# Kernel tuning notes

Measured on AMD Instinct MI355X. Metric: run time of the kernel, lower is better.

Reference implementation:

```python
import jax, jax.numpy as jnp
import numpy as np
import math

B, N, D, H, T = 256, 512, 512, 8, 128
HD = D // H
CLIP = 10.0
CAP = 1.0
NEG = -1.0e9


def setup_inputs() -> dict:
    key = jax.random.key(0)
    ks = jax.random.split(key, 12)
    s = 1.0 / math.sqrt(D)
    return {
        "embeddings": jax.random.normal(ks[0], (B, N, D), jnp.float32),
        "mean_graph_emb": jax.random.normal(ks[1], (B, D), jnp.float32),
        "used_capacity": jax.random.uniform(ks[2], (T, B), jnp.float32),
        "Wk": jax.random.normal(ks[3], (D, D), jnp.float32) * s,
        "Wk_tanh": jax.random.normal(ks[4], (D, D), jnp.float32) * s,
        "Wv": jax.random.normal(ks[5], (D, D), jnp.float32) * s,
        "Wq_context": jax.random.normal(ks[6], (D, D), jnp.float32) * s,
        "Wq_step": jax.random.normal(ks[7], (D + 1, D), jnp.float32) * s,
        "Wout": jax.random.normal(ks[8], (D, D), jnp.float32) * s,
        "prev_a": jax.random.randint(ks[9], (T, B), 0, N, jnp.int32),
        "mask": jax.random.randint(ks[10], (T, B, N), 0, 2, jnp.int32),
    }


def reference(embeddings, mean_graph_emb, used_capacity, Wk, Wk_tanh, Wv,
              Wq_context, Wq_step, Wout, prev_a, mask):
    # Projections (done once per graph embedding, as in get_projections)
    K = (embeddings @ Wk).reshape(B, N, H, HD).transpose(0, 2, 1, 3)      # [B,H,N,hd]
    V = (embeddings @ Wv).reshape(B, N, H, HD).transpose(0, 2, 1, 3)      # [B,H,N,hd]
    K_tanh = embeddings @ Wk_tanh                                          # [B,N,D]
    Q_context = mean_graph_emb @ Wq_context                                # [B,D]

    inv_sqrt_hd = 1.0 / math.sqrt(HD)
    inv_sqrt_d = 1.0 / math.sqrt(D)

    def step(carry, xs):
        prev_t, cap_t, mask_t = xs  # [B], [B], [B,N]
        # get_step_context: gather prev node embedding + remaining capacity
        cur_emb = jnp.take_along_axis(embeddings, prev_t[:, None, None], axis=1)[:, 0]  # [B,D]
        step_ctx = jnp.concatenate([cur_emb, (CAP - cap_t)[:, None]], axis=-1)          # [B,D+1]
        q = Q_context + step_ctx @ Wq_step                                               # [B,D]
        qh = q.reshape(B, H, HD)                                                          # [B,H,hd]
        # decoder MHA, seq_len_q = 1
        logits = jnp.einsum("bhd,bhnd->bhn", qh, K) * inv_sqrt_hd                        # [B,H,N]
        logits = jnp.where(mask_t[:, None, :] == 1, NEG, logits)
        attn = jax.nn.softmax(logits, axis=-1)
        mha = jnp.einsum("bhn,bhnd->bhd", attn, V).reshape(B, D) @ Wout                  # [B,D]
        # single-head tanh-clipped pointer logits
        comp = jnp.einsum("bd,bnd->bn", mha, K_tanh) * inv_sqrt_d                        # [B,N]
        comp = jnp.tanh(comp) * CLIP
        comp = jnp.where(mask_t == 1, NEG, comp)
        p = jax.nn.softmax(comp, axis=-1)                                                # [B,N]
        return carry, p

    _, ps = jax.lax.scan(step, None, (prev_a, used_capacity, mask))  # [T,B,N]
    return ps.transpose(1, 0, 2)  # [B,T,N]
```

## Files before the change

kernel.cpp:

```cpp
#include <hip/hip_runtime.h>
#include <hip/hip_bf16.h>

constexpr int Bb = 256;
constexpr int Nn = 512;
constexpr int Dd = 512;
constexpr int Hh = 8;
constexpr int Tt = 128;
#define NEGF (-1.0e9f)

typedef __attribute__((ext_vector_type(4))) float f32x4;
typedef __attribute__((ext_vector_type(8))) short bf16x8;
typedef __attribute__((ext_vector_type(8))) unsigned short u16x8;

#define AS1 __attribute__((address_space(1)))
#define AS3 __attribute__((address_space(3)))

__device__ __forceinline__ unsigned short f2bf(float f) {
  union { float f; unsigned u; } v; v.f = f;
  unsigned r = v.u + 0x7fffu + ((v.u >> 16) & 1u);
  return (unsigned short)(r >> 16);
}

__device__ __forceinline__ unsigned cvtpk(float lo, float hi) {
  unsigned r;
  asm("v_cvt_pk_bf16_f32 %0, %1, %2" : "=v"(r) : "v"(lo), "v"(hi));
  return r;
}

__device__ __forceinline__ void cast8(const float* __restrict__ src,
                                      unsigned short* __restrict__ dst, int i) {
  const float4* s = (const float4*)src + (size_t)i * 2;
  float4 a = s[0], b = s[1];
  u16x8 o;
  o[0] = f2bf(a.x); o[1] = f2bf(a.y); o[2] = f2bf(a.z); o[3] = f2bf(a.w);
  o[4] = f2bf(b.x); o[5] = f2bf(b.y); o[6] = f2bf(b.z); o[7] = f2bf(b.w);
  ((u16x8*)dst)[i] = o;
}

__global__ void prep_k(const float* __restrict__ emb, const int* __restrict__ mask,
                       const float* __restrict__ Wkt, const float* __restrict__ Wout,
                       const float* __restrict__ mge,
                       const float* __restrict__ Wk, const float* __restrict__ Wv,
                       const float* __restrict__ Wqs, const float* __restrict__ Wqc,
                       unsigned short* __restrict__ embB, unsigned* __restrict__ bits,
                       unsigned short* __restrict__ WktB, unsigned short* __restrict__ WoutB,
                       unsigned short* __restrict__ mgeB,
                       unsigned short* __restrict__ WkT, unsigned short* __restrict__ WvT,
                       unsigned short* __restrict__ WqsT, unsigned short* __restrict__ WqcT) {
  __shared__ float t[32][33];
  int bid = blockIdx.x, tid = threadIdx.x;
  if (bid < 32768) {
    cast8(emb, embB, bid * 256 + tid);
  } else if (bid < 98304) {
    size_t gid = (size_t)(bid - 32768) * 256 + tid;
    int mv = mask[gid];
    unsigned long long bal = __ballot(mv == 1);
    if ((tid & 63) == 0) {
      unsigned tt = (unsigned)(gid >> 17);
      unsigned b = (unsigned)((gid >> 9) & 255);
      unsigned n = (unsigned)(gid & 511);
      unsigned* dst = bits + (((size_t)b * 128 + tt) * 16 + (n >> 5));
      dst[0] = (unsigned)bal;
      dst[1] = (unsigned)(bal >> 32);
    }
  } else if (bid < 98432) {
    cast8(Wkt, WktB, (bid - 98304) * 256 + tid);
  } else if (bid < 98560) {
    cast8(Wout, WoutB, (bid - 98432) * 256 + tid);
  } else if (bid < 98624) {
    cast8(mge, mgeB, (bid - 98560) * 256 + tid);
  } else {
    int vb = bid - 98624;
    int mid = vb >> 8;
    int tile = vb & 255;
    const float* S = (mid == 0) ? Wk : (mid == 1) ? Wv : (mid == 2) ? Wqs : Wqc;
    unsigned short* Dst = (mid == 0) ? WkT : (mid == 1) ? WvT : (mid == 2) ? WqsT : WqcT;
    int r0 = (tile >> 4) * 32, c0 = (tile & 15) * 32;
    int tx = tid & 31, ty = tid >> 5;
#pragma unroll
    for (int yy = 0; yy < 4; ++yy) {
      int r = ty + yy * 8;
      t[r][tx] = S[(size_t)(r0 + r) * 512 + c0 + tx];
    }
    __syncthreads();
#pragma unroll
    for (int yy = 0; yy < 4; ++yy) {
      int c = ty + yy * 8;
      Dst[(size_t)(c0 + c) * 512 + r0 + tx] = f2bf(t[tx][c]);
    }
  }
}

__device__ __forceinline__ void stage_tile(const unsigned short* __restrict__ G, int row0, int k0,
                                           unsigned short* lds_base, int wave, int lane) {
#pragma unroll
  for (int c = 0; c < 4; ++c) {
    int chunk = wave * 4 + c;
    const unsigned short* g = G + (size_t)(row0 + chunk * 8 + (lane >> 3)) * 512 + k0 + (lane & 7) * 8;
    __builtin_amdgcn_global_load_lds((AS1 void*)g, (AS3 void*)(lds_base + chunk * 512), 16, 0, 0);
  }
}

__global__ __launch_bounds__(256, 2)
void wfqc_k(const unsigned short* __restrict__ A0, const unsigned short* __restrict__ BT0,
            unsigned short* __restrict__ C0,
            const unsigned short* __restrict__ A1, const unsigned short* __restrict__ BT1,
            float* __restrict__ C1) {
  __shared__ __align__(16) char lds[32768];
  unsigned short* ldsA = (unsigned short*)lds;
  unsigned short* ldsB = ldsA + 8192;
  int bid = blockIdx.x;
  bool qc = (bid >= 16);
  int lb = qc ? bid - 16 : bid;
  const unsigned short* A = qc ? A1 : A0;
  const unsigned short* BT = qc ? BT1 : BT0;
  int mt = lb >> 2, nt = lb & 3;
  int m0 = mt * 128, n0 = nt * 128;
  int tid = threadIdx.x, lane = tid & 63, w = tid >> 6;
  int wm = w >> 1, wn = w & 1;
  int l15 = lane & 15, l4 = lane >> 4;

  f32x4 acc[4][4] = {};
  for (int k0 = 0; k0 < 512; k0 += 64) {
    stage_tile(A, m0, k0, ldsA, w, lane);
    stage_tile(BT, n0, k0, ldsB, w, lane);
    __syncthreads();
#pragma unroll
    for (int ks = 0; ks < 2; ++ks) {
      bf16x8 fa[4], fb[4];
#pragma unroll
      for (int ii = 0; ii < 4; ++ii)
        fa[ii] = *(const bf16x8*)(ldsA + (wm * 64 + ii * 16 + l15) * 64 + ks * 32 + l4 * 8);
#pragma unroll
      for (int jj = 0; jj < 4; ++jj)
        fb[jj] = *(const bf16x8*)(ldsB + (wn * 64 + jj * 16 + l15) * 64 + ks * 32 + l4 * 8);
#pragma unroll
      for (int ii = 0; ii < 4; ++ii)
#pragma unroll
        for (int jj = 0; jj < 4; ++jj)
          acc[ii][jj] = __builtin_amdgcn_mfma_f32_16x16x32_bf16(fa[ii], fb[jj], acc[ii][jj], 0, 0, 0);
    }
    __syncthreads();
  }
#pragma unroll
  for (int ii = 0; ii < 4; ++ii)
#pragma unroll
    for (int jj = 0; jj < 4; ++jj)
#pragma unroll
      for (int r = 0; r < 4; ++r) {
        int row = m0 + wm * 64 + ii * 16 + l4 * 4 + r;
        int col = n0 + wn * 64 + jj * 16 + l15;
        if (qc) C1[(size_t)row * 512 + col] = acc[ii][jj][r];
        else C0[(size_t)row * 512 + col] = f2bf(acc[ii][jj][r]);
      }
}

template <int MODE>
__global__ __launch_bounds__(256, 2)
void gemm5_k(const unsigned short* __restrict__ A, const unsigned short* __restrict__ BT,
             void* __restrict__ Cout,
             const float* __restrict__ Qc, const float* __restrict__ WqsL,
             const float* __restrict__ capp, const int* __restrict__ prev) {
  __shared__ __align__(16) char lds[32768];
  unsigned short* ldsA = (unsigned short*)lds;
  unsigned short* ldsB = ldsA + 8192;
  int xcd = blockIdx.x & 7, loc = blockIdx.x >> 3;
  int ml = loc >> 2, nt = loc & 3;
  int mt = xcd * 32 + ml;
  int m0 = mt * 128, n0 = nt * 128;
  int tid = threadIdx.x, lane = tid & 63, w = tid >> 6;
  int wm = w >> 1, wn = w & 1;
  int l15 = lane & 15, l4 = lane >> 4;

  const unsigned short* gbase[4];
#pragma unroll
  for (int c = 0; c < 4; ++c) {
    int row = m0 + (w * 4 + c) * 8 + (lane >> 3);
    if (MODE == 3) {
      int t = row >> 8, bb = row & 255;
      int pa = prev[t * Bb + bb];
      gbase[c] = A + (size_t)(bb * 512 + pa) * 512 + (lane & 7) * 8;
    } else {
      gbase[c] = A + (size_t)row * 512 + (lane & 7) * 8;
    }
  }

  f32x4 acc[4][4] = {};
  for (int k0 = 0; k0 < 512; k0 += 64) {
#pragma unroll
    for (int c = 0; c < 4; ++c) {
      int chunk = w * 4 + c;
      __builtin_amdgcn_global_load_lds((AS1 void*)(gbase[c] + k0),
                                       (AS3 void*)(ldsA + chunk * 512), 16, 0, 0);
    }
    stage_tile(BT, n0, k0, ldsB, w, lane);
    __syncthreads();
#pragma unroll
    for (int ks = 0; ks < 2; ++ks) {
      bf16x8 fa[4], fb[4];
#pragma unroll
      for (int ii = 0; ii < 4; ++ii)
        fa[ii] = *(const bf16x8*)(ldsA + (wm * 64 + ii * 16 + l15) * 64 + ks * 32 + l4 * 8);
#pragma unroll
      for (int jj = 0; jj < 4; ++jj)
        fb[jj] = *(const bf16x8*)(ldsB + (wn * 64 + jj * 16 + l15) * 64 + ks * 32 + l4 * 8);
#pragma unroll
      for (int ii = 0; ii < 4; ++ii)
#pragma unroll
        for (int jj = 0; jj < 4; ++jj)
          acc[ii][jj] = __builtin_amdgcn_mfma_f32_16x16x32_bf16(fa[ii], fb[jj], acc[ii][jj], 0, 0, 0);
    }
    __syncthreads();
  }

  if (MODE == 1) {
    unsigned short* C = (unsigned short*)Cout;
#pragma unroll
    for (int ii = 0; ii < 4; ++ii)
#pragma unroll
      for (int jj = 0; jj < 4; ++jj)
#pragma unroll
        for (int r = 0; r < 4; ++r) {
          int row = m0 + wm * 64 + ii * 16 + l4 * 4 + r;
          int col = n0 + wn * 64 + jj * 16 + l15;
          C[(size_t)row * 512 + col] = f2bf(acc[ii][jj][r]);
        }
  } else {
    unsigned short* C = (unsigned short*)Cout;
#pragma unroll
    for (int ii = 0; ii < 4; ++ii)
#pragma unroll
      for (int jj = 0; jj < 4; ++jj)
#pragma unroll
        for (int r = 0; r < 4; ++r) {
          int row = m0 + wm * 64 + ii * 16 + l4 * 4 + r;
          int col = n0 + wn * 64 + jj * 16 + l15;
          int t = row >> 8, bbx = row & 255;
          float val = acc[ii][jj][r] + Qc[(size_t)bbx * 512 + col] + (1.0f - capp[row]) * WqsL[col];
          C[(size_t)(bbx * 128 + t) * 512 + col] = f2bf(val * 0.125f);
        }
  }
}

#define STAGE10A(SLOT, H, ROWB, KT)                                               \
  do {                                                                             \
    int rb_ = (ROWB) + (H) * 128;                                                  \
    char* Lb_ = lds + (SLOT) * 32768 + (H) * 16384;                                \
    _Pragma("unroll")                                                              \
    for (int sh_ = 0; sh_ < 2; ++sh_) {                                            \
      int off_ = sh_ * 8192 + tid * 16;                                            \
      int r_ = off_ >> 7;                                                          \
      int c_ = (off_ & 127) ^ ((r_ & 7) << 4);                                     \
      const char* g_ = (const char*)(A + (size_t)(rb_ + r_) * 512 + (KT) * 64) + c_; \
      __builtin_amdgcn_global_load_lds((AS1 void*)g_, (AS3 void*)(Lb_ + off_), 16, 0, 0); \
    }                                                                              \
  } while (0)

#define STAGE10B(SLOT, H, KT)                                                      \
  do {                                                                             \
    int rb_ = n0 + (H) * 128;                                                      \
    char* Lb_ = lds + 98304 + (SLOT) * 32768 + (H) * 16384;                        \
    _Pragma("unroll")                                                              \
    for (int sh_ = 0; sh_ < 2; ++sh_) {                                            \
      int off_ = sh_ * 8192 + tid * 16;                                            \
      int r_ = off_ >> 7;                                                          \
      int c_ = (off_ & 127) ^ ((r_ & 7) << 4);                                     \
      const char* g_ = (const char*)(BT + (size_t)(rb_ + r_) * 512 + (KT) * 64) + c_; \
      __builtin_amdgcn_global_load_lds((AS1 void*)g_, (AS3 void*)(Lb_ + off_), 16, 0, 0); \
    }                                                                              \
  } while (0)

#define LDA_Q(QM)                                                   \
  _Pragma("unroll")                                                 \
  for (int ii = 0; ii < 4; ++ii) {                                  \
    int rr_ = (QM) * 64 + ii * 16 + l15;                            \
    const char* ap_ = ldsAh + rr_ * 128;                            \
    int sw_ = (rr_ & 7) << 4;                                       \
    fa[ii][0] = *(const bf16x8*)(ap_ + ((l4 * 16) ^ sw_));          \
    fa[ii][1] = *(const bf16x8*)(ap_ + ((64 + l4 * 16) ^ sw_));     \
  }

#define LDB_Q(QN)                                                   \
  _Pragma("unroll")                                                 \
  for (int jj = 0; jj < 2; ++jj) {                                  \
    int rr_ = (wn & 1) * 64 + (QN) * 32 + jj * 16 + l15;            \
    const char* bp_ = ldsBh + rr_ * 128;                            \
    int sw_ = (rr_ & 7) << 4;                                       \
    fb[jj][0] = *(const bf16x8*)(bp_ + ((l4 * 16) ^ sw_));          \
    fb[jj][1] = *(const bf16x8*)(bp_ + ((64 + l4 * 16) ^ sw_));     \
  }

#define MM16(QM, QN)                                                              \
  do {                                                                            \
    __builtin_amdgcn_s_setprio(1);                                                \
    _Pragma("unroll")                                                             \
    for (int ii = 0; ii < 4; ++ii)                                                \
      _Pragma("unroll")                                                           \
      for (int jj = 0; jj < 2; ++jj) {                                            \
        acc[(QM) * 4 + ii][(QN) * 2 + jj] = __builtin_amdgcn_mfma_f32_16x16x32_bf16( \
            fa[ii][0], fb[jj][0], acc[(QM) * 4 + ii][(QN) * 2 + jj], 0, 0, 0);    \
        acc[(QM) * 4 + ii][(QN) * 2 + jj] = __builtin_amdgcn_mfma_f32_16x16x32_bf16( \
            fa[ii][1], fb[jj][1], acc[(QM) * 4 + ii][(QN) * 2 + jj], 0, 0, 0);    \
      }                                                                           \
    __builtin_amdgcn_s_setprio(0);                                                \
  } while (0)

__global__ __launch_bounds__(512, 1)
void gemm10_k(const unsigned short* __restrict__ A,
              const unsigned short* __restrict__ B0, const unsigned short* __restrict__ B1,
              unsigned short* __restrict__ C0, unsigned short* __restrict__ C2) {
  __shared__ __align__(16) char lds[163840];
  int xcd = blockIdx.x & 7, loc = blockIdx.x >> 3;
  int ml4 = loc >> 2, cmb = loc & 3;
  int grp = cmb >> 1, nh = cmb & 1;
  const unsigned short* BT = grp ? B1 : B0;
  int mtb = xcd * 64 + ml4 * 4;
  int n0 = nh * 256;
  int tid = threadIdx.x, lane = tid & 63, w = tid >> 6;
  int wm = w >> 2, wn = w & 3;
  int l15 = lane & 15, l4 = lane >> 4;

  f32x4 acc[8][4] = {};
  bf16x8 fa[4][2], fb[2][2];

  {
    int m00 = mtb * 256;
    STAGE10A(0, 0, m00, 0); STAGE10A(0, 1, m00, 0);
    STAGE10A(1, 0, m00, 1); STAGE10A(1, 1, m00, 1);
    STAGE10B(0, 0, 0);      STAGE10B(0, 1, 0);
  }

  for (int g = 0; g < 32; ++g) {
    int As = g % 3, Astg = (g + 2) % 3;
    int Bs = g & 1, Bstg = Bs ^ 1;
    char* ldsAh = lds + As * 32768 + wm * 16384;
    char* ldsBh = lds + 98304 + Bs * 32768 + (wn >> 1) * 16384;
    int g2 = g + 2;
    int m0A = (mtb + (g2 >> 3)) * 256, ktA = g2 & 7;
    int ktB = (g + 1) & 7;
    if (g < 30) {
      STAGE10A(Astg, 0, m0A, ktA);
      asm volatile("s_waitcnt vmcnt(2)" ::: "memory");
    } else {
      asm volatile("s_waitcnt vmcnt(0)" ::: "memory");
    }
    __builtin_amdgcn_s_barrier();
    LDA_Q(0); LDB_Q(0);
    MM16(0, 0);
    __builtin_amdgcn_s_barrier();
    LDB_Q(1);
    if (g < 30) STAGE10A(Astg, 1, m0A, ktA);
    __builtin_amdgcn_s_barrier();
    MM16(0, 1);
    __builtin_amdgcn_s_barrier();
    LDA_Q(1);
    if (g < 31) STAGE10B(Bstg, 0, ktB);
    __builtin_amdgcn_s_barrier();
    MM16(1, 1);
    __builtin_amdgcn_s_barrier();
    LDB_Q(0);
    if (g < 31) STAGE10B(Bstg, 1, ktB);
    __builtin_amdgcn_s_barrier();
    MM16(1, 0);
    __builtin_amdgcn_s_barrier();

    if ((g & 7) == 7) {
      int m0cur = (mtb + (g >> 3)) * 256;
      if (grp == 0) {
#pragma unroll
        for (int mi = 0; mi < 8; ++mi)
#pragma unroll
          for (int nj = 0; nj < 4; ++nj)
#pragma unroll
            for (int r = 0; r < 4; ++r) {
              int row = m0cur + wm * 128 + mi * 16 + l4 * 4 + r;
              int col = n0 + wn * 64 + nj * 16 + l15;
              C0[(size_t)row * 512 + col] = f2bf(acc[mi][nj][r]);
            }
      } else {
        int bb = m0cur >> 9, nn0 = m0cur & 511;
        char* wb = lds + As * 32768 + w * 4096;
        int rdrow = lane >> 3, nseg = lane & 7;
#pragma unroll
        for (int p = 0; p < 8; ++p) {
          int nj = p >> 1;
          if ((l15 >> 3) == (p & 1)) {
            int rowL = l15 & 7;
#pragma unroll
            for (int mi = 0; mi < 8; ++mi) {
              ushort4 w4;
              w4.x = f2bf(acc[mi][nj][0]);
              w4.y = f2bf(acc[mi][nj][1]);
              w4.z = f2bf(acc[mi][nj][2]);
              w4.w = f2bf(acc[mi][nj][3]);
              *(ushort4*)(wb + rowL * 272 + (mi * 16 + l4 * 4) * 2) = w4;
            }
          }
          asm volatile("s_waitcnt lgkmcnt(0)" ::: "memory");
          u16x8 v0 = *(const u16x8*)(wb + rdrow * 272 + nseg * 16);
          u16x8 v1 = *(const u16x8*)(wb + rdrow * 272 + 128 + nseg * 16);
          int dglob = n0 + wn * 64 + p * 8 + rdrow;
          unsigned short* dp = C2 + (size_t)(bb * 512 + dglob) * 512 + nn0 + wm * 128;
          *(u16x8*)(dp + nseg * 8) = v0;
          *(u16x8*)(dp + 64 + nseg * 8) = v1;
          asm volatile("s_waitcnt lgkmcnt(0)" ::: "memory");
        }
      }
#pragma unroll
      for (int mi = 0; mi < 8; ++mi)
#pragma unroll
        for (int nj = 0; nj < 4; ++nj)
          acc[mi][nj] = (f32x4){0.f, 0.f, 0.f, 0.f};
      __syncthreads();
    }
  }
}

#define STAGEK5(CH, SLOT)                                                          \
  do {                                                                             \
    _Pragma("unroll")                                                              \
    for (int sh_ = 0; sh_ < 2; ++sh_) {                                            \
      int off_ = sh_ * 8192 + tid * 16;                                            \
      int r_ = off_ >> 7;                                                          \
      int c_ = (off_ & 127) ^ ((r_ & 7) << 4);                                     \
      const char* g_ = (const char*)(Kb + (size_t)(b * 512 + (CH) * 128 + r_) * 512 + h * 64) + c_; \
      __builtin_amdgcn_global_load_lds((AS1 void*)g_, (AS3 void*)(lds + (SLOT) * 16384 + off_), 16, 0, 0); \
    }                                                                              \
  } while (0)

#define STAGEV5(CH, SLOT)                                                          \
  do {                                                                             \
    _Pragma("unroll")                                                              \
    for (int sh_ = 0; sh_ < 2; ++sh_) {                                            \
      int off_ = sh_ * 8192 + tid * 16;                                            \
      int r_ = off_ >> 8;                                                          \
      int c_ = (off_ & 255) ^ ((r_ & 7) << 4);                                     \
      const char* g_ = (const char*)(Vt + (size_t)(b * 512 + h * 64 + r_) * 512 + (CH) * 128) + c_; \
      __builtin_amdgcn_global_load_lds((AS1 void*)g_, (AS3 void*)(lds + 32768 + (SLOT) * 16384 + off_), 16, 0, 0); \
    }                                                                              \
  } while (0)

#define CHUNK5(CH)                                                                 \
  do {                                                                             \
    const char* Ks_ = lds + ((CH) & 1) * 16384;                                    \
    const char* Vs_ = lds + 32768 + ((CH) & 1) * 16384;                            \
    f32x4 sck[8];                                                                  \
    _Pragma("unroll")                                                              \
    for (int jj = 0; jj < 8; ++jj) sck[jj] = (f32x4){0.f, 0.f, 0.f, 0.f};          \
    _Pragma("unroll")                                                              \
    for (int jj = 0; jj < 8; ++jj) {                                               \
      int rr_ = jj * 16 + l15;                                                     \
      int sw_ = (rr_ & 7) << 4;                                                    \
      bf16x8 k0_ = *(const bf16x8*)(Ks_ + rr_ * 128 + ((l4 * 16) ^ sw_));          \
      bf16x8 k1_ = *(const bf16x8*)(Ks_ + rr_ * 128 + ((64 + l4 * 16) ^ sw_));     \
      sck[jj] = __builtin_amdgcn_mfma_f32_16x16x32_bf16(k0_, fq[0], sck[jj], 0, 0, 0); \
      sck[jj] = __builtin_amdgcn_mfma_f32_16x16x32_bf16(k1_, fq[1], sck[jj], 0, 0, 0); \
    }                                                                              \
    unsigned mwarr_[4] = {mqs[CH].x, mqs[CH].y, mqs[CH].z, mqs[CH].w};             \
    float cmx_ = -3.0e38f;                                                         \
    _Pragma("unroll")                                                              \
    for (int jj = 0; jj < 8; ++jj) {                                               \
      unsigned nib_ = mwarr_[jj >> 1] >> (((jj & 1) << 4) + (l4 << 2));            \
      _Pragma("unroll")                                                            \
      for (int r = 0; r < 4; ++r)                                                  \
        sck[jj][r] = ((nib_ >> r) & 1) ? NEGF : sck[jj][r];                        \
      float m01_ = fmaxf(sck[jj][0], sck[jj][1]);                                  \
      float m23_ = fmaxf(sck[jj][2], sck[jj][3]);                                  \
      cmx_ = fmaxf(cmx_, fmaxf(m01_, m23_));                                       \
    }                                                                              \
    cmx_ = fmaxf(cmx_, __shfl_xor(cmx_, 16));                                      \
    cmx_ = fmaxf(cmx_, __shfl_xor(cmx_, 32));                                      \
    float mn_ = fmaxf(mx, cmx_);                                                   \
    float al_ = __expf(mx - mn_);                                                  \
    sum *= al_;                                                                    \
    _Pragma("unroll")                                                              \
    for (int dj = 0; dj < 4; ++dj)                                                 \
      _Pragma("unroll")                                                            \
      for (int r = 0; r < 4; ++r) o[dj][r] *= al_;                                 \
    mx = mn_;                                                                      \
    _Pragma("unroll")                                                              \
    for (int jj = 0; jj < 8; ++jj) {                                               \
      _Pragma("unroll")                                                            \
      for (int r = 0; r < 4; ++r) sck[jj][r] = __expf(sck[jj][r] - mx);            \
      sum += (sck[jj][0] + sck[jj][1]) + (sck[jj][2] + sck[jj][3]);                \
    }                                                                              \
    _Pragma("unroll")                                                              \
    for (int g = 0; g < 4; ++g) {                                                  \
      unsigned a0_ = cvtpk(sck[2 * g][0], sck[2 * g][1]);                          \
      unsigned a1_ = cvtpk(sck[2 * g][2], sck[2 * g][3]);                          \
      unsigned b0_ = cvtpk(sck[2 * g + 1][0], sck[2 * g + 1][1]);                  \
      unsigned b1_ = cvtpk(sck[2 * g + 1][2], sck[2 * g + 1][3]);                  \
      unsigned wA0_ = __shfl(a0_, src0, 64), wB0_ = __shfl(b0_, src0, 64);         \
      unsigned wA1_ = __shfl(a1_, src0, 64), wB1_ = __shfl(b1_, src0, 64);         \
      unsigned wA2_ = __shfl(a0_, src2, 64), wB2_ = __shfl(b0_, src2, 64);         \
      unsigned wA3_ = __shfl(a1_, src2, 64), wB3_ = __shfl(b1_, src2, 64);         \
      union { unsigned u[4]; bf16x8 v; } pu_;                                      \
      pu_.u[0] = loh ? wA0_ : wB0_;                                                \
      pu_.u[1] = loh ? wA1_ : wB1_;                                                \
      pu_.u[2] = loh ? wA2_ : wB2_;                                                \
      pu_.u[3] = loh ? wA3_ : wB3_;                                                \
      _Pragma("unroll")                                                            \
      for (int dj = 0; dj < 4; ++dj) {                                             \
        int rr_ = dj * 16 + l15;                                                   \
        int sw_ = (rr_ & 7) << 4;                                                  \
        bf16x8 fv_ = *(const bf16x8*)(Vs_ + rr_ * 256 + ((g * 64 + l4 * 16) ^ sw_)); \
        o[dj] = __builtin_amdgcn_mfma_f32_16x16x32_bf16(fv_, pu_.v, o[dj], 0, 0, 0); \
      }                                                                            \
    }                                                                              \
  } while (0)

__global__ __launch_bounds__(512, 4)
void attn5_k(const unsigned short* __restrict__ Qb, const unsigned short* __restrict__ Kb,
             const unsigned short* __restrict__ Vt, const unsigned* __restrict__ mbits,
             unsigned short* __restrict__ mhaB) {
  __shared__ __align__(16) char lds[65536];
  int bid = blockIdx.x;
  int h = bid & 7, b = bid >> 3;
  int tid = threadIdx.x, lane = tid & 63, w = tid >> 6;
  int l15 = lane & 15, l4 = lane >> 4;
  int t = w * 16 + l15;

  bf16x8 fq[2];
#pragma unroll
  for (int ks = 0; ks < 2; ++ks)
    fq[ks] = *(const bf16x8*)(Qb + (size_t)(b * 128 + t) * 512 + h * 64 + ks * 32 + l4 * 8);
  uint4 mqs[4];
  {
    const uint4* mp = (const uint4*)(mbits + (((size_t)b * 128 + t) << 4));
    mqs[0] = mp[0]; mqs[1] = mp[1]; mqs[2] = mp[2]; mqs[3] = mp[3];
  }

  float mx = -3.0e38f, sum = 0.f;
  f32x4 o[4] = {};
  int src0 = l15 + ((l4 & 1) ? 32 : 0);
  int src2 = l15 + ((l4 & 1) ? 48 : 16);
  bool loh = (l4 < 2);

  STAGEK5(0, 0); STAGEV5(0, 0);
  STAGEK5(1, 1); STAGEV5(1, 1);
  asm volatile("s_waitcnt vmcnt(4)" ::: "memory");
  __builtin_amdgcn_s_barrier();
  CHUNK5(0);
  __builtin_amdgcn_s_barrier();
  STAGEK5(2, 0); STAGEV5(2, 0);
  asm volatile("s_waitcnt vmcnt(4)" ::: "memory");
  __builtin_amdgcn_s_barrier();
  CHUNK5(1);
  __builtin_amdgcn_s_barrier();
  STAGEK5(3, 1); STAGEV5(3, 1);
  asm volatile("s_waitcnt vmcnt(4)" ::: "memory");
  __builtin_amdgcn_s_barrier();
  CHUNK5(2);
  __builtin_amdgcn_s_barrier();
  asm volatile("s_waitcnt vmcnt(0)" ::: "memory");
  __builtin_amdgcn_s_barrier();
  CHUNK5(3);

  sum += __shfl_xor(sum, 16);
  sum += __shfl_xor(sum, 32);
  float inv = 1.0f / sum;
#pragma unroll
  for (int dj = 0; dj < 4; ++dj) {
    ushort4 w4;
    w4.x = f2bf(o[dj][0] * inv);
    w4.y = f2bf(o[dj][1] * inv);
    w4.z = f2bf(o[dj][2] * inv);
    w4.w = f2bf(o[dj][3] * inv);
    *(ushort4*)(mhaB + (size_t)(b * 128 + t) * 512 + h * 64 + dj * 16 + l4 * 4) = w4;
  }
}

#define STAGEC5(CH, SLOT)                                                          \
  do {                                                                             \
    _Pragma("unroll")                                                              \
    for (int ps_ = 0; ps_ < 4; ++ps_) {                                            \
      int off_ = ps_ * 8192 + tid * 16;                                            \
      int r_ = off_ >> 10;                                                         \
      int c_ = (off_ & 1023) ^ ((r_ & 7) << 4);                                    \
      const char* g_ = (const char*)(embB + (size_t)(b * 512 + nh * 256 + (CH) * 32 + r_) * 512) + c_; \
      __builtin_amdgcn_global_load_lds((AS1 void*)g_, (AS3 void*)(lds + (SLOT) * 32768 + off_), 16, 0, 0); \
    }                                                                              \
  } while (0)

#define CCHUNK5(CH)                                                                \
  do {                                                                             \
    const char* Es_ = lds + ((CH) & 1) * 32768;                                    \
    _Pragma("unroll")                                                              \
    for (int jjl_ = 0; jjl_ < 2; ++jjl_) {                                         \
      f32x4 sck = (f32x4){0.f, 0.f, 0.f, 0.f};                                     \
      int rr_ = jjl_ * 16 + l15;                                                   \
      const char* ep_ = Es_ + rr_ * 1024;                                          \
      int sw_ = (rr_ & 7) << 4;                                                    \
      _Pragma("unroll")                                                            \
      for (int ks_ = 0; ks_ < 16; ++ks_) {                                         \
        bf16x8 fa_ = *(const bf16x8*)(ep_ + ((ks_ * 64 + l4 * 16) ^ sw_));         \
        sck = __builtin_amdgcn_mfma_f32_16x16x32_bf16(fa_, fb[ks_], sck, 0, 0, 0); \
      }                                                                            \
      unsigned nib_ = mwh[CH] >> ((jjl_ << 4) + (l4 << 2));                        \
      float4 o4_;                                                                  \
      float* po_ = (float*)&o4_;                                                   \
      _Pragma("unroll")                                                            \
      for (int r = 0; r < 4; ++r) {                                                \
        float y_ = sck[r] * 0.044194173824159216f;                                 \
        y_ = fminf(fmaxf(y_, -15.f), 15.f);                                        \
        float e2_ = __expf(2.f * y_);                                              \
        float th_ = (e2_ - 1.f) / (e2_ + 1.f);                                     \
        float p_ = __expf(th_ * 10.f - 10.f);                                      \
        p_ = ((nib_ >> r) & 1) ? 0.f : p_;                                         \
        po_[r] = p_;                                                               \
        sum += p_;                                                                 \
      }                                                                            \
      *(float4*)(out + (size_t)(b * 128 + t) * 512 + nh * 256 + (CH) * 32 + jjl_ * 16 + l4 * 4) = o4_; \
    }                                                                              \
  } while (0)

__global__ __launch_bounds__(512, 2)
void comp5_k(const unsigned short* __restrict__ mh2, const unsigned short* __restrict__ embB,
             const unsigned* __restrict__ mbits, float* __restrict__ out,
             float* __restrict__ sums) {
  __shared__ __align__(16) char lds[65536];
  int b = blockIdx.x >> 1, nh = blockIdx.x & 1;
  int tid = threadIdx.x, lane = tid & 63, w = tid >> 6;
  int l15 = lane & 15, l4 = lane >> 4;
  int t = w * 16 + l15;

  bf16x8 fb[16];
#pragma unroll
  for (int ks = 0; ks < 16; ++ks)
    fb[ks] = *(const bf16x8*)(mh2 + (size_t)(b * 128 + t) * 512 + ks * 32 + l4 * 8);
  unsigned mwh[8];
  {
    const uint4* mp = (const uint4*)(mbits + (((size_t)b * 128 + t) << 4)) + nh * 2;
    uint4 a0 = mp[0], a1 = mp[1];
    mwh[0] = a0.x; mwh[1] = a0.y; mwh[2] = a0.z; mwh[3] = a0.w;
    mwh[4] = a1.x; mwh[5] = a1.y; mwh[6] = a1.z; mwh[7] = a1.w;
  }

  float sum = 0.f;
  STAGEC5(0, 0);
  STAGEC5(1, 1);
  asm volatile("s_waitcnt vmcnt(4)" ::: "memory");
  __builtin_amdgcn_s_barrier();
  CCHUNK5(0);
  __builtin_amdgcn_s_barrier();
  STAGEC5(2, 0);
  asm volatile("s_waitcnt vmcnt(4)" ::: "memory");
  __builtin_amdgcn_s_barrier();
  CCHUNK5(1);
  __builtin_amdgcn_s_barrier();
  STAGEC5(3, 1);
  asm volatile("s_waitcnt vmcnt(4)" ::: "memory");
  __builtin_amdgcn_s_barrier();
  CCHUNK5(2);
  __builtin_amdgcn_s_barrier();
  STAGEC5(4, 0);
  asm volatile("s_waitcnt vmcnt(4)" ::: "memory");
  __builtin_amdgcn_s_barrier();
  CCHUNK5(3);
  __builtin_amdgcn_s_barrier();
  STAGEC5(5, 1);
  asm volatile("s_waitcnt vmcnt(4)" ::: "memory");
  __builtin_amdgcn_s_barrier();
  CCHUNK5(4);
  __builtin_amdgcn_s_barrier();
  STAGEC5(6, 0);
  asm volatile("s_waitcnt vmcnt(4)" ::: "memory");
  __builtin_amdgcn_s_barrier();
  CCHUNK5(5);
  __builtin_amdgcn_s_barrier();
  STAGEC5(7, 1);
  asm volatile("s_waitcnt vmcnt(4)" ::: "memory");
  __builtin_amdgcn_s_barrier();
  CCHUNK5(6);
  __builtin_amdgcn_s_barrier();
  asm volatile("s_waitcnt vmcnt(0)" ::: "memory");
  __builtin_amdgcn_s_barrier();
  CCHUNK5(7);

  sum += __shfl_xor(sum, 16);
  sum += __shfl_xor(sum, 32);
  if (l4 == 0) sums[nh * 32768 + b * 128 + t] = sum;
}

__global__ void norm_k(float* __restrict__ out, const float* __restrict__ sums) {
  int row = blockIdx.x * 4 + (threadIdx.x >> 6);
  int lane = threadIdx.x & 63;
  float inv = 1.0f / (sums[row] + sums[32768 + row]);
  float4* p = (float4*)(out + (size_t)row * 512) + lane;
  float4 a = p[0], b = p[64];
  a.x *= inv; a.y *= inv; a.z *= inv; a.w *= inv;
  b.x *= inv; b.y *= inv; b.z *= inv; b.w *= inv;
  p[0] = a; p[64] = b;
}

extern "C" void kernel_launch(void* const* d_in, const int* in_sizes, int n_in,
                              void* d_out, int out_size, void* d_ws, size_t ws_size,
                              hipStream_t stream) {
  (void)in_sizes; (void)n_in; (void)out_size; (void)ws_size;
  const float* emb  = (const float*)d_in[0];
  const float* mge  = (const float*)d_in[1];
  const float* cap  = (const float*)d_in[2];
  const float* Wk   = (const float*)d_in[3];
  const float* Wkt  = (const float*)d_in[4];
  const float* Wv   = (const float*)d_in[5];
  const float* Wqc  = (const float*)d_in[6];
  const float* Wqs  = (const float*)d_in[7];
  const float* Wout = (const float*)d_in[8];
  const int* prev   = (const int*)d_in[9];
  const int* mask   = (const int*)d_in[10];
  float* out = (float*)d_out;

  char* p = (char*)d_ws;
  auto take = [&](size_t n) { char* q = p; p += (n + 255) & ~(size_t)255; return q; };
  unsigned short* embB = (unsigned short*)take((size_t)131072 * 512 * 2);
  unsigned short* Kb   = (unsigned short*)take((size_t)131072 * 512 * 2);
  unsigned short* Vt   = (unsigned short*)take((size_t)131072 * 512 * 2);
  unsigned short* Qb   = (unsigned short*)take((size_t)32768 * 512 * 2);
  unsigned short* mhaB = (unsigned short*)take((size_t)32768 * 512 * 2);
  unsigned short* mh2  = (unsigned short*)take((size_t)32768 * 512 * 2);
  float*          Qc   = (float*)take((size_t)256 * 512 * 4);
  unsigned*       mbit = (unsigned*)take((size_t)256 * 128 * 16 * 4);
  float*          sums = (float*)take((size_t)2 * 32768 * 4);
  unsigned short* WkT  = (unsigned short*)take(524288);
  unsigned short* WvT  = (unsigned short*)take(524288);
  unsigned short* WqsT = (unsigned short*)take(524288);
  unsigned short* WqcT = (unsigned short*)take(524288);
  unsigned short* WktB = (unsigned short*)take(524288);
  unsigned short* WoutB= (unsigned short*)take(524288);
  unsigned short* WFT  = (unsigned short*)take(524288);
  unsigned short* mgeB = (unsigned short*)take((size_t)256 * 512 * 2);

  prep_k<<<99648, 256, 0, stream>>>(emb, mask, Wkt, Wout, mge, Wk, Wv, Wqs, Wqc,
                                    embB, mbit, WktB, WoutB, mgeB, WkT, WvT, WqsT, WqcT);
  wfqc_k<<<24, 256, 0, stream>>>(WktB, WoutB, WFT, mgeB, WqcT, Qc);
  gemm5_k<3><<<1024, 256, 0, stream>>>(embB, WqsT, Qb, Qc, Wqs + 512 * 512, cap, prev);
  gemm10_k<<<512, 512, 0, stream>>>(embB, WkT, WvT, Kb, Vt);
  attn5_k<<<2048, 512, 0, stream>>>(Qb, Kb, Vt, mbit, mhaB);
  gemm5_k<1><<<1024, 256, 0, stream>>>(mhaB, WFT, mh2, nullptr, nullptr, nullptr, nullptr);
  comp5_k<<<512, 512, 0, stream>>>(mh2, embB, mbit, out, sums);
  norm_k<<<8192, 256, 0, stream>>>(out, sums);
}
```

Before: 510.9 us.

## Replace 128x128 GEMMs with 256x256 double-buffered swizzled-LDS GEMM kernel

Both the gathered query-projection GEMM and the mha·WF GEMM move from a 128x128-tile, 4-wave, single-buffered kernel to a 256x256-tile, 8-wave kernel. The new kernel double-buffers LDS, uses XOR-swizzled layouts, and interleaves staging of the next K slice with MFMA quadrants between barriers. The aim is more operand reuse per loaded byte and hiding global-load latency behind MFMA work. In exchange it uses 128KB of LDS at one block per CU, and only 256 blocks are launched, which may leave some CUs underused.

```diff
diff --git a/kernel.cpp b/kernel.cpp
--- a/kernel.cpp
+++ b/kernel.cpp
@@ -155,121 +155,6 @@
       }
 }
 
-template <int MODE>
-__global__ __launch_bounds__(256, 2)
-void gemm5_k(const unsigned short* __restrict__ A, const unsigned short* __restrict__ BT,
-             void* __restrict__ Cout,
-             const float* __restrict__ Qc, const float* __restrict__ WqsL,
-             const float* __restrict__ capp, const int* __restrict__ prev) {
-  __shared__ __align__(16) char lds[32768];
-  unsigned short* ldsA = (unsigned short*)lds;
-  unsigned short* ldsB = ldsA + 8192;
-  int xcd = blockIdx.x & 7, loc = blockIdx.x >> 3;
-  int ml = loc >> 2, nt = loc & 3;
-  int mt = xcd * 32 + ml;
-  int m0 = mt * 128, n0 = nt * 128;
-  int tid = threadIdx.x, lane = tid & 63, w = tid >> 6;
-  int wm = w >> 1, wn = w & 1;
-  int l15 = lane & 15, l4 = lane >> 4;
-
-  const unsigned short* gbase[4];
-#pragma unroll
-  for (int c = 0; c < 4; ++c) {
-    int row = m0 + (w * 4 + c) * 8 + (lane >> 3);
-    if (MODE == 3) {
-      int t = row >> 8, bb = row & 255;
-      int pa = prev[t * Bb + bb];
-      gbase[c] = A + (size_t)(bb * 512 + pa) * 512 + (lane & 7) * 8;
-    } else {
-      gbase[c] = A + (size_t)row * 512 + (lane & 7) * 8;
-    }
-  }
-
-  f32x4 acc[4][4] = {};
-  for (int k0 = 0; k0 < 512; k0 += 64) {
-#pragma unroll
-    for (int c = 0; c < 4; ++c) {
-      int chunk = w * 4 + c;
-      __builtin_amdgcn_global_load_lds((AS1 void*)(gbase[c] + k0),
-                                       (AS3 void*)(ldsA + chunk * 512), 16, 0, 0);
-    }
-    stage_tile(BT, n0, k0, ldsB, w, lane);
-    __syncthreads();
-#pragma unroll
-    for (int ks = 0; ks < 2; ++ks) {
-      bf16x8 fa[4], fb[4];
-#pragma unroll
-      for (int ii = 0; ii < 4; ++ii)
-        fa[ii] = *(const bf16x8*)(ldsA + (wm * 64 + ii * 16 + l15) * 64 + ks * 32 + l4 * 8);
-#pragma unroll
-      for (int jj = 0; jj < 4; ++jj)
-        fb[jj] = *(const bf16x8*)(ldsB + (wn * 64 + jj * 16 + l15) * 64 + ks * 32 + l4 * 8);
-#pragma unroll
-      for (int ii = 0; ii < 4; ++ii)
-#pragma unroll
-        for (int jj = 0; jj < 4; ++jj)
-          acc[ii][jj] = __builtin_amdgcn_mfma_f32_16x16x32_bf16(fa[ii], fb[jj], acc[ii][jj], 0, 0, 0);
-    }
-    __syncthreads();
-  }
-
-  if (MODE == 1) {
-    unsigned short* C = (unsigned short*)Cout;
-#pragma unroll
-    for (int ii = 0; ii < 4; ++ii)
-#pragma unroll
-      for (int jj = 0; jj < 4; ++jj)
-#pragma unroll
-        for (int r = 0; r < 4; ++r) {
-          int row = m0 + wm * 64 + ii * 16 + l4 * 4 + r;
-          int col = n0 + wn * 64 + jj * 16 + l15;
-          C[(size_t)row * 512 + col] = f2bf(acc[ii][jj][r]);
-        }
-  } else {
-    unsigned short* C = (unsigned short*)Cout;
-#pragma unroll
-    for (int ii = 0; ii < 4; ++ii)
-#pragma unroll
-      for (int jj = 0; jj < 4; ++jj)
-#pragma unroll
-        for (int r = 0; r < 4; ++r) {
-          int row = m0 + wm * 64 + ii * 16 + l4 * 4 + r;
-          int col = n0 + wn * 64 + jj * 16 + l15;
-          int t = row >> 8, bbx = row & 255;
-          float val = acc[ii][jj][r] + Qc[(size_t)bbx * 512 + col] + (1.0f - capp[row]) * WqsL[col];
-          C[(size_t)(bbx * 128 + t) * 512 + col] = f2bf(val * 0.125f);
-        }
-  }
-}
-
-#define STAGE10A(SLOT, H, ROWB, KT)                                               \
-  do {                                                                             \
-    int rb_ = (ROWB) + (H) * 128;                                                  \
-    char* Lb_ = lds + (SLOT) * 32768 + (H) * 16384;                                \
-    _Pragma("unroll")                                                              \
-    for (int sh_ = 0; sh_ < 2; ++sh_) {                                            \
-      int off_ = sh_ * 8192 + tid * 16;                                            \
-      int r_ = off_ >> 7;                                                          \
-      int c_ = (off_ & 127) ^ ((r_ & 7) << 4);                                     \
-      const char* g_ = (const char*)(A + (size_t)(rb_ + r_) * 512 + (KT) * 64) + c_; \
-      __builtin_amdgcn_global_load_lds((AS1 void*)g_, (AS3 void*)(Lb_ + off_), 16, 0, 0); \
-    }                                                                              \
-  } while (0)
-
-#define STAGE10B(SLOT, H, KT)                                                      \
-  do {                                                                             \
-    int rb_ = n0 + (H) * 128;                                                      \
-    char* Lb_ = lds + 98304 + (SLOT) * 32768 + (H) * 16384;                        \
-    _Pragma("unroll")                                                              \
-    for (int sh_ = 0; sh_ < 2; ++sh_) {                                            \
-      int off_ = sh_ * 8192 + tid * 16;                                            \
-      int r_ = off_ >> 7;                                                          \
-      int c_ = (off_ & 127) ^ ((r_ & 7) << 4);                                     \
-      const char* g_ = (const char*)(BT + (size_t)(rb_ + r_) * 512 + (KT) * 64) + c_; \
-      __builtin_amdgcn_global_load_lds((AS1 void*)g_, (AS3 void*)(Lb_ + off_), 16, 0, 0); \
-    }                                                                              \
-  } while (0)
-
 #define LDA_Q(QM)                                                   \
   _Pragma("unroll")                                                 \
   for (int ii = 0; ii < 4; ++ii) {                                  \
@@ -303,6 +188,34 @@
             fa[ii][1], fb[jj][1], acc[(QM) * 4 + ii][(QN) * 2 + jj], 0, 0, 0);    \
       }                                                                           \
     __builtin_amdgcn_s_setprio(0);                                                \
+  } while (0)
+
+#define STAGE10A(SLOT, H, ROWB, KT)                                               \
+  do {                                                                             \
+    int rb_ = (ROWB) + (H) * 128;                                                  \
+    char* Lb_ = lds + (SLOT) * 32768 + (H) * 16384;                                \
+    _Pragma("unroll")                                                              \
+    for (int sh_ = 0; sh_ < 2; ++sh_) {                                            \
+      int off_ = sh_ * 8192 + tid * 16;                                            \
+      int r_ = off_ >> 7;                                                          \
+      int c_ = (off_ & 127) ^ ((r_ & 7) << 4);                                     \
+      const char* g_ = (const char*)(A + (size_t)(rb_ + r_) * 512 + (KT) * 64) + c_; \
+      __builtin_amdgcn_global_load_lds((AS1 void*)g_, (AS3 void*)(Lb_ + off_), 16, 0, 0); \
+    }                                                                              \
+  } while (0)
+
+#define STAGE10B(SLOT, H, KT)                                                      \
+  do {                                                                             \
+    int rb_ = n0 + (H) * 128;                                                      \
+    char* Lb_ = lds + 98304 + (SLOT) * 32768 + (H) * 16384;                        \
+    _Pragma("unroll")                                                              \
+    for (int sh_ = 0; sh_ < 2; ++sh_) {                                            \
+      int off_ = sh_ * 8192 + tid * 16;                                            \
+      int r_ = off_ >> 7;                                                          \
+      int c_ = (off_ & 127) ^ ((r_ & 7) << 4);                                     \
+      const char* g_ = (const char*)(BT + (size_t)(rb_ + r_) * 512 + (KT) * 64) + c_; \
+      __builtin_amdgcn_global_load_lds((AS1 void*)g_, (AS3 void*)(Lb_ + off_), 16, 0, 0); \
+    }                                                                              \
   } while (0)
 
 __global__ __launch_bounds__(512, 1)
@@ -413,6 +326,124 @@
           acc[mi][nj] = (f32x4){0.f, 0.f, 0.f, 0.f};
       __syncthreads();
     }
+  }
+}
+
+#define STAGE11A(SLOT, H, KT)                                                      \
+  do {                                                                             \
+    char* Lb_ = lds + (SLOT) * 65536 + (H) * 16384;                                \
+    __builtin_amdgcn_global_load_lds((AS1 void*)(abase[(H) * 2 + 0] + (KT) * 128), \
+        (AS3 void*)(Lb_ + tid * 16), 16, 0, 0);                                    \
+    __builtin_amdgcn_global_load_lds((AS1 void*)(abase[(H) * 2 + 1] + (KT) * 128), \
+        (AS3 void*)(Lb_ + 8192 + tid * 16), 16, 0, 0);                             \
+  } while (0)
+
+#define STAGE11B(SLOT, H, KT)                                                      \
+  do {                                                                             \
+    int rb_ = n0 + (H) * 128;                                                      \
+    char* Lb_ = lds + (SLOT) * 65536 + 32768 + (H) * 16384;                        \
+    _Pragma("unroll")                                                              \
+    for (int sh_ = 0; sh_ < 2; ++sh_) {                                            \
+      int off_ = sh_ * 8192 + tid * 16;                                            \
+      int r_ = off_ >> 7;                                                          \
+      int c_ = (off_ & 127) ^ ((r_ & 7) << 4);                                     \
+      const char* g_ = (const char*)(BT + (size_t)(rb_ + r_) * 512 + (KT) * 64) + c_; \
+      __builtin_amdgcn_global_load_lds((AS1 void*)g_, (AS3 void*)(Lb_ + off_), 16, 0, 0); \
+    }                                                                              \
+  } while (0)
+
+template <int MODE>
+__global__ __launch_bounds__(512, 1)
+void gemm11_k(const unsigned short* __restrict__ A, const unsigned short* __restrict__ BT,
+              unsigned short* __restrict__ C,
+              const float* __restrict__ Qc, const float* __restrict__ WqsL,
+              const float* __restrict__ capp, const int* __restrict__ prev) {
+  __shared__ __align__(16) char lds[131072];
+  int xcd = blockIdx.x & 7, loc = blockIdx.x >> 3;
+  int mt = xcd * 16 + (loc >> 1), nh = loc & 1;
+  int m0 = mt * 256, n0 = nh * 256;
+  int tid = threadIdx.x, lane = tid & 63, w = tid >> 6;
+  int wm = w >> 2, wn = w & 3;
+  int l15 = lane & 15, l4 = lane >> 4;
+
+  const char* abase[4];
+#pragma unroll
+  for (int hs = 0; hs < 4; ++hs) {
+    int H = hs >> 1, sh = hs & 1;
+    int off = sh * 8192 + tid * 16;
+    int r = off >> 7;
+    int c = (off & 127) ^ ((r & 7) << 4);
+    int row = m0 + H * 128 + r;
+    if (MODE == 3) {
+      int t = row >> 8, bb = row & 255;
+      int pa = prev[t * Bb + bb];
+      abase[hs] = (const char*)(A + (size_t)(bb * 512 + pa) * 512) + c;
+    } else {
+      abase[hs] = (const char*)(A + (size_t)row * 512) + c;
+    }
+  }
+
+  f32x4 acc[8][4] = {};
+  bf16x8 fa[4][2], fb[2][2];
+
+  STAGE11A(0, 0, 0); STAGE11A(0, 1, 0);
+  STAGE11B(0, 0, 0); STAGE11B(0, 1, 0);
+
+  for (int kt = 0; kt < 8; ++kt) {
+    int s = kt & 1, sn = s ^ 1;
+    char* ldsAh = lds + s * 65536 + wm * 16384;
+    char* ldsBh = lds + s * 65536 + 32768 + (wn >> 1) * 16384;
+    if (kt < 7) {
+      STAGE11A(sn, 0, kt + 1);
+      asm volatile("s_waitcnt vmcnt(2)" ::: "memory");
+    } else {
+      asm volatile("s_waitcnt vmcnt(0)" ::: "memory");
+    }
+    __builtin_amdgcn_s_barrier();
+    LDA_Q(0); LDB_Q(0);
+    MM16(0, 0);
+    __builtin_amdgcn_s_barrier();
+    LDB_Q(1);
+    if (kt < 7) STAGE11A(sn, 1, kt + 1);
+    __builtin_amdgcn_s_barrier();
+    MM16(0, 1);
+    __builtin_amdgcn_s_barrier();
+    LDA_Q(1);
+    if (kt < 7) STAGE11B(sn, 0, kt + 1);
+    __builtin_amdgcn_s_barrier();
+    MM16(1, 1);
+    __builtin_amdgcn_s_barrier();
+    LDB_Q(0);
+    if (kt < 7) STAGE11B(sn, 1, kt + 1);
+    __builtin_amdgcn_s_barrier();
+    MM16(1, 0);
+    __builtin_amdgcn_s_barrier();
+  }
+
+  if (MODE == 1) {
+#pragma unroll
+    for (int mi = 0; mi < 8; ++mi)
+#pragma unroll
+      for (int nj = 0; nj < 4; ++nj)
+#pragma unroll
+        for (int r = 0; r < 4; ++r) {
+          int row = m0 + wm * 128 + mi * 16 + l4 * 4 + r;
+          int col = n0 + wn * 64 + nj * 16 + l15;
+          C[(size_t)row * 512 + col] = f2bf(acc[mi][nj][r]);
+        }
+  } else {
+#pragma unroll
+    for (int mi = 0; mi < 8; ++mi)
+#pragma unroll
+      for (int nj = 0; nj < 4; ++nj)
+#pragma unroll
+        for (int r = 0; r < 4; ++r) {
+          int row = m0 + wm * 128 + mi * 16 + l4 * 4 + r;
+          int col = n0 + wn * 64 + nj * 16 + l15;
+          int t = row >> 8, bbx = row & 255;
+          float val = acc[mi][nj][r] + Qc[(size_t)bbx * 512 + col] + (1.0f - capp[row]) * WqsL[col];
+          C[(size_t)(bbx * 128 + t) * 512 + col] = f2bf(val * 0.125f);
+        }
   }
 }
 
@@ -733,10 +764,10 @@
   prep_k<<<99648, 256, 0, stream>>>(emb, mask, Wkt, Wout, mge, Wk, Wv, Wqs, Wqc,
                                     embB, mbit, WktB, WoutB, mgeB, WkT, WvT, WqsT, WqcT);
   wfqc_k<<<24, 256, 0, stream>>>(WktB, WoutB, WFT, mgeB, WqcT, Qc);
-  gemm5_k<3><<<1024, 256, 0, stream>>>(embB, WqsT, Qb, Qc, Wqs + 512 * 512, cap, prev);
+  gemm11_k<3><<<256, 512, 0, stream>>>(embB, WqsT, Qb, Qc, Wqs + 512 * 512, cap, prev);
   gemm10_k<<<512, 512, 0, stream>>>(embB, WkT, WvT, Kb, Vt);
   attn5_k<<<2048, 512, 0, stream>>>(Qb, Kb, Vt, mbit, mhaB);
-  gemm5_k<1><<<1024, 256, 0, stream>>>(mhaB, WFT, mh2, nullptr, nullptr, nullptr, nullptr);
+  gemm11_k<1><<<256, 512, 0, stream>>>(mhaB, WFT, mh2, nullptr, nullptr, nullptr, nullptr);
   comp5_k<<<512, 512, 0, stream>>>(mh2, embB, mbit, out, sums);
   norm_k<<<8192, 256, 0, stream>>>(out, sums);
 }
```

Result: faster. 492.1 us (-3.7%).
